# Performance work log

Hardware: AMD Instinct MI355X
Metric: run time of the kernel (lower is better)

Reference implementation:

```python
import jax, jax.numpy as jnp
import numpy as np

N = 100000; E = 1600000; G = 512; L = 1000
FXD = 4; FXT = 5; H = 64; NOUT = 2

def setup_inputs() -> dict:
    key = jax.random.key(0)
    ks = jax.random.split(key, 16)
    x = jax.random.normal(ks[0], (N, FXD), dtype=jnp.float32)
    edge_index = jax.random.randint(ks[1], (2, E), 0, N, dtype=jnp.int64)
    # contiguous, non-empty graph assignment (sorted)
    batch = jnp.minimum(jnp.arange(N, dtype=jnp.int64) // (N // G), G - 1)
    target = jax.random.normal(ks[2], (G, L, FXT), dtype=jnp.float32)
    def lin(k, fi, fo):
        s = 1.0 / np.sqrt(fi)
        k1, k2 = jax.random.split(k)
        return (jax.random.uniform(k1, (fi, fo), jnp.float32, -s, s),
                jax.random.uniform(k2, (fo,), jnp.float32, -s, s))
    W1, b1 = lin(ks[3], FXD, H)
    W2, b2 = lin(ks[4], H, 2 * H)
    Wg, bg = lin(ks[5], 2 * H, H)
    s = 1.0 / np.sqrt(FXT * 3)
    Wc = jax.random.uniform(ks[6], (H, FXT, 3), jnp.float32, -s, s)  # OIH
    bc = jax.random.uniform(ks[7], (H,), jnp.float32, -s, s)
    Wt, bt = lin(ks[8], H, H)
    Wf, bf = lin(ks[9], 2 * H, H)
    Wo, bo = lin(ks[10], H, NOUT)
    return dict(x=x, edge_index=edge_index, batch=batch, target=target,
                W1=W1, b1=b1, W2=W2, b2=b2, Wg=Wg, bg=bg,
                Wc=Wc, bc=bc, Wt=Wt, bt=bt, Wf=Wf, bf=bf, Wo=Wo, bo=bo)

def _gcn_prep(edge_index):
    # add self-loops, compute symmetric normalization (PyG gcn_norm)
    loops = jnp.arange(N, dtype=edge_index.dtype)
    row = jnp.concatenate([edge_index[0], loops])
    col = jnp.concatenate([edge_index[1], loops])
    deg = jax.ops.segment_sum(jnp.ones_like(col, dtype=jnp.float32), col, num_segments=N)
    dis = jnp.where(deg > 0, jax.lax.rsqrt(deg), 0.0)
    norm = dis[row] * dis[col]  # [E+N]
    return row, col, norm

def _gcn_conv(h, row, col, norm):
    # gather-scale-scatter aggregation
    msg = h[row] * norm[:, None]
    return jax.ops.segment_sum(msg, col, num_segments=N)

def reference(x, edge_index, batch, target, W1, b1, W2, b2, Wg, bg, Wc, bc, Wt, bt, Wf, bf, Wo, bo):
    row, col, norm = _gcn_prep(edge_index)
    h = jax.nn.relu(_gcn_conv(x @ W1, row, col, norm) + b1)
    h = jax.nn.relu(_gcn_conv(h @ W2, row, col, norm) + b2)
    g = jax.ops.segment_max(h, batch, num_segments=G)  # global_max_pool [G, 2H]
    g = g @ Wg + bg  # dropout = identity (eval)
    t = jnp.transpose(target, (0, 2, 1))  # [G, FXT, L]
    t = jax.lax.conv_general_dilated(t, Wc, (1,), 'VALID',
                                     dimension_numbers=('NCH', 'OIH', 'NCH')) + bc[None, :, None]
    t = jax.nn.relu(t)
    t = jnp.max(t, axis=-1)  # AdaptiveMaxPool1d(1) [G, H]
    t = t @ Wt + bt
    xc = jnp.concatenate([g, t], axis=1)
    xc = jax.nn.relu(xc @ Wf + bf)
    return xc @ Wo + bo
```

## Files before the change

### kernel.cpp

```cpp
#include <hip/hip_runtime.h>
#include <hip/hip_bf16.h>

constexpr int N   = 100000;
constexpr int E   = 1600000;
constexpr int G   = 512;
constexpr int L   = 1000;
constexpr int NPG = 195;

constexpr int SLOTS = 48;
constexpr int NR2   = 256;
constexpr int RS2   = 391;
constexpr int PCAP2 = 6912;
constexpr int BCH   = 4096;
constexpr int NBP   = (E + BCH - 1) / BCH;

typedef __attribute__((ext_vector_type(8))) short bf16x8;
typedef __attribute__((ext_vector_type(4))) float f32x4;

__device__ __forceinline__ float bf2f(__hip_bfloat16 b) { return __bfloat162float(b); }
__device__ __forceinline__ float lo_bf(unsigned v) { return __uint_as_float(v << 16); }
__device__ __forceinline__ float hi_bf(unsigned v) { return __uint_as_float(v & 0xFFFF0000u); }
__device__ __forceinline__ unsigned packbf2(float a, float b) {
    __hip_bfloat16 ha = __float2bfloat16(a), hb = __float2bfloat16(b);
    unsigned short ua = *(unsigned short*)&ha, ub = *(unsigned short*)&hb;
    return (unsigned)ua | ((unsigned)ub << 16);
}

struct SMPart { unsigned rec[BCH]; unsigned char rr[BCH];
                int cnt[NR2]; int base[NR2]; int cur[NR2]; };
struct SMConv { float tg[L * 5]; float pm[4 * 64]; };


__global__ void __launch_bounds__(256) k_part_conv(
        const int* __restrict__ row, const int* __restrict__ col,
        int* __restrict__ pcnt, unsigned* __restrict__ precs,
        const float* __restrict__ target, const float* __restrict__ Wc,
        const float* __restrict__ bc, float* __restrict__ tb,
        const float* __restrict__ W2, short* __restrict__ W2hi,
        short* __restrict__ W2lo) {
    __shared__ __align__(16) char smbuf[sizeof(SMPart) > sizeof(SMConv)
                                        ? sizeof(SMPart) : sizeof(SMConv)];
    int tid = threadIdx.x;
    int bid = blockIdx.x;
    if (bid < NBP) {
        SMPart& sp = *reinterpret_cast<SMPart*>(smbuf);
        sp.cnt[tid] = 0;
        __syncthreads();
        int e0 = bid * BCH;
        int nE = min(BCH, E - e0);
        for (int i = tid; i < nE; i += 256) {
            int c = __builtin_nontemporal_load(col + e0 + i);
            int r = __builtin_nontemporal_load(row + e0 + i);
            int rr = c / RS2;
            sp.rec[i] = ((unsigned)r << 9) | (unsigned)(c - rr * RS2);
            sp.rr[i] = (unsigned char)rr;
            atomicAdd(&sp.cnt[rr], 1);
        }
        __syncthreads();
        sp.base[tid] = atomicAdd(&pcnt[tid], sp.cnt[tid]);
        sp.cur[tid] = 0;
        __syncthreads();
        for (int i = tid; i < nE; i += 256) {
            int rr = sp.rr[i];
            int p = sp.base[rr] + atomicAdd(&sp.cur[rr], 1);
            if (p < PCAP2) precs[rr * PCAP2 + p] = sp.rec[i];
        }
    } else if (bid < NBP + G) {
        SMConv& sc = *reinterpret_cast<SMConv*>(smbuf);
        int gi = bid - NBP;
        const float* tsrc = target + (size_t)gi * (L * 5);
        for (int i = tid; i < L * 5; i += 256) sc.tg[i] = tsrc[i];
        __syncthreads();
        int co = tid & 63, rr = tid >> 6;
        float wc[15];
        #pragma unroll
        for (int j = 0; j < 15; j++) wc[j] = Wc[co * 15 + j];
        const float* tg = sc.tg;
        int p0 = rr * 250;
        int pend = min(p0 + 250, 998);
        float a0 = tg[p0 * 5 + 0], a1 = tg[p0 * 5 + 1], a2 = tg[p0 * 5 + 2],
              a3 = tg[p0 * 5 + 3], a4 = tg[p0 * 5 + 4];
        float b0 = tg[p0 * 5 + 5], b1 = tg[p0 * 5 + 6], b2 = tg[p0 * 5 + 7],
              b3 = tg[p0 * 5 + 8], b4 = tg[p0 * 5 + 9];
        float m = -1e30f;
        for (int p = p0; p < pend; p++) {
            const float* cp = &tg[(p + 2) * 5];
            float c0 = cp[0], c1 = cp[1], c2 = cp[2], c3 = cp[3], c4 = cp[4];
            float v = 0.0f;
            v = fmaf(a0, wc[0],  v); v = fmaf(b0, wc[1],  v); v = fmaf(c0, wc[2],  v);
            v = fmaf(a1, wc[3],  v); v = fmaf(b1, wc[4],  v); v = fmaf(c1, wc[5],  v);
            v = fmaf(a2, wc[6],  v); v = fmaf(b2, wc[7],  v); v = fmaf(c2, wc[8],  v);
            v = fmaf(a3, wc[9],  v); v = fmaf(b3, wc[10], v); v = fmaf(c3, wc[11], v);
            v = fmaf(a4, wc[12], v); v = fmaf(b4, wc[13], v); v = fmaf(c4, wc[14], v);
            m = fmaxf(m, v);
            a0 = b0; a1 = b1; a2 = b2; a3 = b3; a4 = b4;
            b0 = c0; b1 = c1; b2 = c2; b3 = c3; b4 = c4;
        }
        sc.pm[rr * 64 + co] = m;
        __syncthreads();
        if (tid < 64) {
            float mm = fmaxf(fmaxf(sc.pm[tid], sc.pm[64 + tid]),
                             fmaxf(sc.pm[128 + tid], sc.pm[192 + tid]));
            tb[gi * 64 + tid] = fmaxf(mm + bc[tid], 0.0f);
        }
    } else {
        int i = (bid - NBP - G) * 256 + tid;
        if (i < 64 * 128) {
            float w = W2[i];
            __hip_bfloat16 h = __float2bfloat16(w);
            float r = w - __bfloat162float(h);
            __hip_bfloat16 l = __float2bfloat16(r);
            W2hi[i] = *(short*)&h;
            W2lo[i] = *(short*)&l;
        }
    }
}


__global__ void __launch_bounds__(256) k_sort(
        const int* __restrict__ pcnt, const unsigned* __restrict__ precs,
        int* __restrict__ slots, int* __restrict__ cursor, float* __restrict__ dis) {
    __shared__ unsigned recs[PCAP2];
    __shared__ int hist[512], off[512], off2[512], ps[256];
    int tid = threadIdx.x;
    int rr = blockIdx.x;
    int cnt = min(pcnt[rr], PCAP2);
    hist[tid] = 0; hist[tid + 256] = 0;
    __syncthreads();
    const unsigned* pr = precs + rr * PCAP2;
    for (int i = tid; i < cnt; i += 256) {
        unsigned r = pr[i];
        recs[i] = r;
        atomicAdd(&hist[r & 511], 1);
    }
    __syncthreads();
    int h0 = hist[2 * tid], h1 = hist[2 * tid + 1];
    int s = h0 + h1;
    ps[tid] = s;
    __syncthreads();
    for (int d = 1; d < 256; d <<= 1) {
        int v = (tid >= d) ? ps[tid - d] : 0;
        __syncthreads();
        ps[tid] += v;
        __syncthreads();
    }
    int excl = ps[tid] - s;
    off[2 * tid] = excl;       off[2 * tid + 1] = excl + h0;
    off2[2 * tid] = excl;      off2[2 * tid + 1] = excl + h0;
    __syncthreads();
    for (int ln = tid; ln < RS2; ln += 256) {
        int n = rr * RS2 + ln;
        if (n < N) {
            int c = hist[ln];
            dis[n] = rsqrtf((float)c + 1.0f);
            cursor[n] = n * SLOTS + min(c, SLOTS);
        }
    }
    for (int i = tid; i < cnt; i += 256) {
        unsigned r = recs[i];
        int ln = (int)(r & 511u);
        int p = atomicAdd(&off2[ln], 1);
        int j = p - off[ln];
        if (j < SLOTS) slots[(rr * RS2 + ln) * SLOTS + j] = (int)(r >> 9);
    }
}


__global__ void __launch_bounds__(256) k_gxl1(
        const int* __restrict__ cursor, const int* __restrict__ slots,
        const float* __restrict__ dis, const float4* __restrict__ x,
        const float* __restrict__ W1, const float* __restrict__ b1,
        unsigned* __restrict__ h32) {
    __shared__ float ax[256][4];
    __shared__ float w1s[256];
    __shared__ float b1s[64];
    int tid = threadIdx.x;
    w1s[tid] = W1[tid];
    if (tid < 64) b1s[tid] = b1[tid];
    int nb = blockIdx.x * 256;
    int n = nb + tid;
    float4 a = make_float4(0.f, 0.f, 0.f, 0.f);
    if (n < N) {
        int s = n * SLOTS;
        int cnt = cursor[n] - s;
        float dn = dis[n];
        int j = 0;
        for (; j + 4 <= cnt; j += 4) {
            int s0 = slots[s + j], s1 = slots[s + j + 1],
                s2 = slots[s + j + 2], s3 = slots[s + j + 3];
            float w0 = dis[s0], w1 = dis[s1], w2 = dis[s2], w3 = dis[s3];
            float4 v0 = x[s0], v1 = x[s1], v2 = x[s2], v3 = x[s3];
            a.x = fmaf(v0.x, w0, a.x); a.y = fmaf(v0.y, w0, a.y);
            a.z = fmaf(v0.z, w0, a.z); a.w = fmaf(v0.w, w0, a.w);
            a.x = fmaf(v1.x, w1, a.x); a.y = fmaf(v1.y, w1, a.y);
            a.z = fmaf(v1.z, w1, a.z); a.w = fmaf(v1.w, w1, a.w);
            a.x = fmaf(v2.x, w2, a.x); a.y = fmaf(v2.y, w2, a.y);
            a.z = fmaf(v2.z, w2, a.z); a.w = fmaf(v2.w, w2, a.w);
            a.x = fmaf(v3.x, w3, a.x); a.y = fmaf(v3.y, w3, a.y);
            a.z = fmaf(v3.z, w3, a.z); a.w = fmaf(v3.w, w3, a.w);
        }
        for (; j < cnt; j++) {
            int sx = slots[s + j];
            float w = dis[sx];
            float4 v = x[sx];
            a.x = fmaf(v.x, w, a.x); a.y = fmaf(v.y, w, a.y);
            a.z = fmaf(v.z, w, a.z); a.w = fmaf(v.w, w, a.w);
        }
        float4 xs = x[n];
        float sl = dn * dn;
        a.x = fmaf(xs.x, sl, a.x * dn);
        a.y = fmaf(xs.y, sl, a.y * dn);
        a.z = fmaf(xs.z, sl, a.z * dn);
        a.w = fmaf(xs.w, sl, a.w * dn);
    }
    ax[tid][0] = a.x; ax[tid][1] = a.y; ax[tid][2] = a.z; ax[tid][3] = a.w;
    __syncthreads();
    int p = tid & 31, r0 = tid >> 5;
    int f0 = 2 * p, f1 = 2 * p + 1;
    float wA0 = w1s[f0],       wB0 = w1s[f1];
    float wA1 = w1s[64 + f0],  wB1 = w1s[64 + f1];
    float wA2 = w1s[128 + f0], wB2 = w1s[128 + f1];
    float wA3 = w1s[192 + f0], wB3 = w1s[192 + f1];
    float bb0 = b1s[f0], bb1 = b1s[f1];
    #pragma unroll 4
    for (int i = 0; i < 32; i++) {
        int ln = r0 + 8 * i;
        int node = nb + ln;
        if (node >= N) break;
        float v0 = bb0, v1 = bb1;
        float g0 = ax[ln][0], g1 = ax[ln][1], g2 = ax[ln][2], g3 = ax[ln][3];
        v0 = fmaf(g0, wA0, v0); v1 = fmaf(g0, wB0, v1);
        v0 = fmaf(g1, wA1, v0); v1 = fmaf(g1, wB1, v1);
        v0 = fmaf(g2, wA2, v0); v1 = fmaf(g2, wB2, v1);
        v0 = fmaf(g3, wA3, v0); v1 = fmaf(g3, wB3, v1);
        h32[(size_t)node * 32 + p] = packbf2(fmaxf(v0, 0.0f), fmaxf(v1, 0.0f));
    }
}


__global__ void __launch_bounds__(256) k_gather_h(
        const int* __restrict__ cursor, const int* __restrict__ slots,
        const float* __restrict__ dis, const unsigned* __restrict__ h32,
        unsigned* __restrict__ aggh32) {
    __shared__ int2 lsw[8][SLOTS];
    __shared__ int  lcnt[8];
    int tid = threadIdx.x;
    int nb = blockIdx.x * 8;
    if (tid < 8) {
        int node = nb + tid;
        lcnt[tid] = (node < N) ? (cursor[node] - node * SLOTS) : 0;
    }
    __syncthreads();
    for (int i = tid; i < 8 * SLOTS; i += 256) {
        int lo = i / SLOTS, j = i - lo * SLOTS;
        if (j < lcnt[lo]) {
            int src = slots[(nb + lo) * SLOTS + j];
            lsw[lo][j] = make_int2(src, __float_as_int(dis[src]));
        }
    }
    __syncthreads();
    int wid = tid >> 6, lane = tid & 63;
    int half = lane >> 5, li = lane & 31;
    int local = wid * 2 + half;
    int n = nb + local;
    if (n >= N) return;
    int cnt = lcnt[local];
    float dn = dis[n];
    float acc0 = 0.0f, acc1 = 0.0f;
    int j = 0;
    for (; j + 16 <= cnt; j += 16) {
        unsigned v[16]; float w[16];
        #pragma unroll
        for (int k = 0; k < 16; k++) {
            int2 e = lsw[local][j + k];
            v[k] = h32[(size_t)e.x * 32 + li];
            w[k] = __int_as_float(e.y);
        }
        #pragma unroll
        for (int k = 0; k < 16; k++) {
            acc0 = fmaf(w[k], lo_bf(v[k]), acc0);
            acc1 = fmaf(w[k], hi_bf(v[k]), acc1);
        }
    }
    for (; j + 4 <= cnt; j += 4) {
        unsigned v[4]; float w[4];
        #pragma unroll
        for (int k = 0; k < 4; k++) {
            int2 e = lsw[local][j + k];
            v[k] = h32[(size_t)e.x * 32 + li];
            w[k] = __int_as_float(e.y);
        }
        #pragma unroll
        for (int k = 0; k < 4; k++) {
            acc0 = fmaf(w[k], lo_bf(v[k]), acc0);
            acc1 = fmaf(w[k], hi_bf(v[k]), acc1);
        }
    }
    for (; j < cnt; j++) {
        int2 e = lsw[local][j];
        unsigned v = h32[(size_t)e.x * 32 + li];
        float w = __int_as_float(e.y);
        acc0 = fmaf(w, lo_bf(v), acc0);
        acc1 = fmaf(w, hi_bf(v), acc1);
    }
    unsigned sv = h32[(size_t)n * 32 + li];
    acc0 = fmaf(dn, lo_bf(sv), acc0) * dn;
    acc1 = fmaf(dn, hi_bf(sv), acc1) * dn;
    aggh32[(size_t)n * 32 + li] = packbf2(acc0, acc1);
}


__global__ void __launch_bounds__(256) k_mfma_pool(
        const __hip_bfloat16* __restrict__ aggh,
        const short* __restrict__ W2hi, const short* __restrict__ W2lo,
        const float* __restrict__ b2, const float* __restrict__ tb,
        const float* __restrict__ Wg, const float* __restrict__ bg,
        const float* __restrict__ Wt, const float* __restrict__ bt,
        const float* __restrict__ Wf, const float* __restrict__ bf,
        const float* __restrict__ Wo, const float* __restrict__ bo,
        float* __restrict__ out) {
    __shared__ float gvec[128], ts[64], g2s[64], t2s[64], xcs[64];
    int tid = threadIdx.x;
    int wid = tid >> 6, lane = tid & 63;
    int m = lane & 15, quad = lane >> 4;
    int gi = blockIdx.x;
    int n0 = gi * NPG;
    int n1 = (gi == G - 1) ? N : n0 + NPG;
    int cb0 = wid * 32, cb1 = cb0 + 16;
    bf16x8 bh[2][2], bl[2][2];
    #pragma unroll
    for (int t = 0; t < 2; t++) {
        int cb = cb0 + t * 16;
        #pragma unroll
        for (int ks = 0; ks < 2; ks++) {
            bf16x8 hh, ll;
            #pragma unroll
            for (int j = 0; j < 8; j++) {
                int k = ks * 32 + quad * 8 + j;
                hh[j] = W2hi[k * 128 + cb + m];
                ll[j] = W2lo[k * 128 + cb + m];
            }
            bh[t][ks] = hh; bl[t][ks] = ll;
        }
    }
    float bias0 = b2[cb0 + m], bias1 = b2[cb1 + m];
    const short* ah = (const short*)aggh;
    float mx0 = 0.0f, mx1 = 0.0f;
    bf16x8 a0, a1;
    {
        const short* p = ah + (size_t)(n0 + m) * 64 + quad * 8;
        a0 = *(const bf16x8*)p;
        a1 = *(const bf16x8*)(p + 32);
    }
    for (int bn = n0; bn < n1; bn += 16) {
        bf16x8 na0 = a0, na1 = a1;
        if (bn + 16 < n1) {
            const short* p = ah + (size_t)(bn + 16 + m) * 64 + quad * 8;
            na0 = *(const bf16x8*)p;
            na1 = *(const bf16x8*)(p + 32);
        }
        f32x4 acc0 = {0.f, 0.f, 0.f, 0.f};
        f32x4 acc1 = {0.f, 0.f, 0.f, 0.f};
        acc0 = __builtin_amdgcn_mfma_f32_16x16x32_bf16(a0, bh[0][0], acc0, 0, 0, 0);
        acc0 = __builtin_amdgcn_mfma_f32_16x16x32_bf16(a1, bh[0][1], acc0, 0, 0, 0);
        acc0 = __builtin_amdgcn_mfma_f32_16x16x32_bf16(a0, bl[0][0], acc0, 0, 0, 0);
        acc0 = __builtin_amdgcn_mfma_f32_16x16x32_bf16(a1, bl[0][1], acc0, 0, 0, 0);
        acc1 = __builtin_amdgcn_mfma_f32_16x16x32_bf16(a0, bh[1][0], acc1, 0, 0, 0);
        acc1 = __builtin_amdgcn_mfma_f32_16x16x32_bf16(a1, bh[1][1], acc1, 0, 0, 0);
        acc1 = __builtin_amdgcn_mfma_f32_16x16x32_bf16(a0, bl[1][0], acc1, 0, 0, 0);
        acc1 = __builtin_amdgcn_mfma_f32_16x16x32_bf16(a1, bl[1][1], acc1, 0, 0, 0);
        int rb = bn + quad * 4;
        #pragma unroll
        for (int r = 0; r < 4; r++) {
            float v0 = fmaxf(acc0[r] + bias0, 0.0f);
            float v1 = fmaxf(acc1[r] + bias1, 0.0f);
            if (rb + r < n1) {
                mx0 = fmaxf(mx0, v0);
                mx1 = fmaxf(mx1, v1);
            }
        }
        a0 = na0; a1 = na1;
    }
    mx0 = fmaxf(mx0, __shfl_xor(mx0, 16));
    mx0 = fmaxf(mx0, __shfl_xor(mx0, 32));
    mx1 = fmaxf(mx1, __shfl_xor(mx1, 16));
    mx1 = fmaxf(mx1, __shfl_xor(mx1, 32));
    if (quad == 0) {
        gvec[cb0 + m] = mx0;
        gvec[cb1 + m] = mx1;
    }
    __syncthreads();
    if (wid == 0) {
        ts[lane] = tb[gi * 64 + lane];
        float a = bg[lane];
        #pragma unroll 8
        for (int k = 0; k < 128; k++) a = fmaf(gvec[k], Wg[k * 64 + lane], a);
        float b = bt[lane];
        #pragma unroll 8
        for (int k = 0; k < 64; k++) b = fmaf(ts[k], Wt[k * 64 + lane], b);
        g2s[lane] = a;
        t2s[lane] = b;
        float c = bf[lane];
        #pragma unroll 8
        for (int k = 0; k < 64; k++) c = fmaf(g2s[k], Wf[k * 64 + lane], c);
        #pragma unroll 8
        for (int k = 0; k < 64; k++) c = fmaf(t2s[k], Wf[(64 + k) * 64 + lane], c);
        xcs[lane] = fmaxf(c, 0.0f);
        if (lane < 2) {
            float o = bo[lane];
            for (int k = 0; k < 64; k++) o = fmaf(xcs[k], Wo[k * 2 + lane], o);
            out[gi * 2 + lane] = o;
        }
    }
}


extern "C" void kernel_launch(void* const* d_in, const int* in_sizes, int n_in,
                              void* d_out, int out_size, void* d_ws, size_t ws_size,
                              hipStream_t stream) {
    const float* x      = (const float*)d_in[0];
    const int*   ei     = (const int*)d_in[1];
    const float* target = (const float*)d_in[3];
    const float* W1 = (const float*)d_in[4];
    const float* b1 = (const float*)d_in[5];
    const float* W2 = (const float*)d_in[6];
    const float* b2 = (const float*)d_in[7];
    const float* Wg = (const float*)d_in[8];
    const float* bg = (const float*)d_in[9];
    const float* Wc = (const float*)d_in[10];
    const float* bc = (const float*)d_in[11];
    const float* Wt = (const float*)d_in[12];
    const float* bt = (const float*)d_in[13];
    const float* Wf = (const float*)d_in[14];
    const float* bf = (const float*)d_in[15];
    const float* Wo = (const float*)d_in[16];
    const float* bo = (const float*)d_in[17];
    float* out = (float*)d_out;

    const int* row = ei;
    const int* col = ei + E;

    char* base = (char*)d_ws;
    size_t o = 0;
    auto alloc = [&](size_t bytes) -> void* {
        void* p = base + o;
        o = (o + bytes + 255) & ~(size_t)255;
        return p;
    };
    int*      cursor = (int*)     alloc((size_t)N * 4);
    float*    dis    = (float*)   alloc((size_t)N * 4);
    int*      slots  = (int*)     alloc((size_t)N * SLOTS * 4);
    int*      pcnt   = (int*)     alloc(NR2 * 4);
    unsigned* precs  = (unsigned*)alloc((size_t)NR2 * PCAP2 * 4);
    __hip_bfloat16* h    = (__hip_bfloat16*)alloc((size_t)N * 64 * 2);
    __hip_bfloat16* aggh = (__hip_bfloat16*)alloc((size_t)N * 64 * 2);
    short*    W2hi   = (short*)   alloc((size_t)64 * 128 * 2);
    short*    W2lo   = (short*)   alloc((size_t)64 * 128 * 2);
    float*    tb     = (float*)   alloc((size_t)G * 64 * 4);
    (void)    alloc(4096);

    (void)hipMemsetAsync(pcnt, 0, NR2 * 4, stream);
    k_part_conv<<<NBP + G + 32, 256, 0, stream>>>(row, col, pcnt, precs,
                                                  target, Wc, bc, tb,
                                                  W2, W2hi, W2lo);
    k_sort     <<<NR2, 256, 0, stream>>>(pcnt, precs, slots, cursor, dis);
    k_gxl1     <<<(N + 255) / 256, 256, 0, stream>>>(cursor, slots, dis,
                                                     (const float4*)x, W1, b1,
                                                     (unsigned*)h);
    k_gather_h <<<(N + 7) / 8, 256, 0, stream>>>(cursor, slots, dis,
                                                 (const unsigned*)h, (unsigned*)aggh);
    k_mfma_pool<<<G, 256, 0, stream>>>(aggh, W2hi, W2lo, b2, tb, Wg, bg, Wt, bt,
                                       Wf, bf, Wo, bo, out);
}
```

Before: 237.6 us.

## Simplify bucket sort to atomic slot fill and split layer-1 gather across 4 lanes

k_sort drops its LDS record staging, histogram prefix scan and second pass, and instead writes slots directly using a per-node atomic counter. The order of neighbours within a slot list now depends on atomic ordering, so floating-point summation order can vary between runs. k_gxl1 now assigns four threads per node, with each lane striding over the neighbour list, and combines the partial sums with xor shuffles. This gives four times as many blocks and is meant to shorten the serial per-thread gather and improve memory-level parallelism.

```diff
diff --git a/kernel.cpp b/kernel.cpp
--- a/kernel.cpp
+++ b/kernel.cpp
@@ -120,48 +120,27 @@
 __global__ void __launch_bounds__(256) k_sort(
         const int* __restrict__ pcnt, const unsigned* __restrict__ precs,
         int* __restrict__ slots, int* __restrict__ cursor, float* __restrict__ dis) {
-    __shared__ unsigned recs[PCAP2];
-    __shared__ int hist[512], off[512], off2[512], ps[256];
+    __shared__ int cnt2[RS2];
     int tid = threadIdx.x;
     int rr = blockIdx.x;
     int cnt = min(pcnt[rr], PCAP2);
-    hist[tid] = 0; hist[tid + 256] = 0;
+    for (int i = tid; i < RS2; i += 256) cnt2[i] = 0;
     __syncthreads();
     const unsigned* pr = precs + rr * PCAP2;
     for (int i = tid; i < cnt; i += 256) {
         unsigned r = pr[i];
-        recs[i] = r;
-        atomicAdd(&hist[r & 511], 1);
-    }
-    __syncthreads();
-    int h0 = hist[2 * tid], h1 = hist[2 * tid + 1];
-    int s = h0 + h1;
-    ps[tid] = s;
-    __syncthreads();
-    for (int d = 1; d < 256; d <<= 1) {
-        int v = (tid >= d) ? ps[tid - d] : 0;
-        __syncthreads();
-        ps[tid] += v;
-        __syncthreads();
-    }
-    int excl = ps[tid] - s;
-    off[2 * tid] = excl;       off[2 * tid + 1] = excl + h0;
-    off2[2 * tid] = excl;      off2[2 * tid + 1] = excl + h0;
+        int ln = (int)(r & 511u);
+        int j = atomicAdd(&cnt2[ln], 1);
+        if (j < SLOTS) slots[(rr * RS2 + ln) * SLOTS + j] = (int)(r >> 9);
+    }
     __syncthreads();
     for (int ln = tid; ln < RS2; ln += 256) {
         int n = rr * RS2 + ln;
         if (n < N) {
-            int c = hist[ln];
+            int c = cnt2[ln];
             dis[n] = rsqrtf((float)c + 1.0f);
             cursor[n] = n * SLOTS + min(c, SLOTS);
         }
-    }
-    for (int i = tid; i < cnt; i += 256) {
-        unsigned r = recs[i];
-        int ln = (int)(r & 511u);
-        int p = atomicAdd(&off2[ln], 1);
-        int j = p - off[ln];
-        if (j < SLOTS) slots[(rr * RS2 + ln) * SLOTS + j] = (int)(r >> 9);
     }
 }
 
@@ -171,49 +150,40 @@
         const float* __restrict__ dis, const float4* __restrict__ x,
         const float* __restrict__ W1, const float* __restrict__ b1,
         unsigned* __restrict__ h32) {
-    __shared__ float ax[256][4];
+    __shared__ float ax[64][4];
     __shared__ float w1s[256];
     __shared__ float b1s[64];
     int tid = threadIdx.x;
     w1s[tid] = W1[tid];
     if (tid < 64) b1s[tid] = b1[tid];
-    int nb = blockIdx.x * 256;
-    int n = nb + tid;
+    int nb = blockIdx.x * 64;
+    int ln = tid >> 2, sub = tid & 3;
+    int n = nb + ln;
     float4 a = make_float4(0.f, 0.f, 0.f, 0.f);
     if (n < N) {
         int s = n * SLOTS;
         int cnt = cursor[n] - s;
-        float dn = dis[n];
-        int j = 0;
-        for (; j + 4 <= cnt; j += 4) {
-            int s0 = slots[s + j], s1 = slots[s + j + 1],
-                s2 = slots[s + j + 2], s3 = slots[s + j + 3];
-            float w0 = dis[s0], w1 = dis[s1], w2 = dis[s2], w3 = dis[s3];
-            float4 v0 = x[s0], v1 = x[s1], v2 = x[s2], v3 = x[s3];
-            a.x = fmaf(v0.x, w0, a.x); a.y = fmaf(v0.y, w0, a.y);
-            a.z = fmaf(v0.z, w0, a.z); a.w = fmaf(v0.w, w0, a.w);
-            a.x = fmaf(v1.x, w1, a.x); a.y = fmaf(v1.y, w1, a.y);
-            a.z = fmaf(v1.z, w1, a.z); a.w = fmaf(v1.w, w1, a.w);
-            a.x = fmaf(v2.x, w2, a.x); a.y = fmaf(v2.y, w2, a.y);
-            a.z = fmaf(v2.z, w2, a.z); a.w = fmaf(v2.w, w2, a.w);
-            a.x = fmaf(v3.x, w3, a.x); a.y = fmaf(v3.y, w3, a.y);
-            a.z = fmaf(v3.z, w3, a.z); a.w = fmaf(v3.w, w3, a.w);
-        }
-        for (; j < cnt; j++) {
+        for (int j = sub; j < cnt; j += 4) {
             int sx = slots[s + j];
             float w = dis[sx];
             float4 v = x[sx];
             a.x = fmaf(v.x, w, a.x); a.y = fmaf(v.y, w, a.y);
             a.z = fmaf(v.z, w, a.z); a.w = fmaf(v.w, w, a.w);
         }
+    }
+    a.x += __shfl_xor(a.x, 1); a.y += __shfl_xor(a.y, 1);
+    a.z += __shfl_xor(a.z, 1); a.w += __shfl_xor(a.w, 1);
+    a.x += __shfl_xor(a.x, 2); a.y += __shfl_xor(a.y, 2);
+    a.z += __shfl_xor(a.z, 2); a.w += __shfl_xor(a.w, 2);
+    if (sub == 0 && n < N) {
+        float dn = dis[n];
+        float sl = dn * dn;
         float4 xs = x[n];
-        float sl = dn * dn;
-        a.x = fmaf(xs.x, sl, a.x * dn);
-        a.y = fmaf(xs.y, sl, a.y * dn);
-        a.z = fmaf(xs.z, sl, a.z * dn);
-        a.w = fmaf(xs.w, sl, a.w * dn);
-    }
-    ax[tid][0] = a.x; ax[tid][1] = a.y; ax[tid][2] = a.z; ax[tid][3] = a.w;
+        ax[ln][0] = fmaf(xs.x, sl, a.x * dn);
+        ax[ln][1] = fmaf(xs.y, sl, a.y * dn);
+        ax[ln][2] = fmaf(xs.z, sl, a.z * dn);
+        ax[ln][3] = fmaf(xs.w, sl, a.w * dn);
+    }
     __syncthreads();
     int p = tid & 31, r0 = tid >> 5;
     int f0 = 2 * p, f1 = 2 * p + 1;
@@ -222,13 +192,13 @@
     float wA2 = w1s[128 + f0], wB2 = w1s[128 + f1];
     float wA3 = w1s[192 + f0], wB3 = w1s[192 + f1];
     float bb0 = b1s[f0], bb1 = b1s[f1];
-    #pragma unroll 4
-    for (int i = 0; i < 32; i++) {
-        int ln = r0 + 8 * i;
-        int node = nb + ln;
+    #pragma unroll
+    for (int i = 0; i < 8; i++) {
+        int l2 = r0 + 8 * i;
+        int node = nb + l2;
         if (node >= N) break;
         float v0 = bb0, v1 = bb1;
-        float g0 = ax[ln][0], g1 = ax[ln][1], g2 = ax[ln][2], g3 = ax[ln][3];
+        float g0 = ax[l2][0], g1 = ax[l2][1], g2 = ax[l2][2], g3 = ax[l2][3];
         v0 = fmaf(g0, wA0, v0); v1 = fmaf(g0, wB0, v1);
         v0 = fmaf(g1, wA1, v0); v1 = fmaf(g1, wB1, v1);
         v0 = fmaf(g2, wA2, v0); v1 = fmaf(g2, wB2, v1);
@@ -464,9 +434,9 @@
                                                   target, Wc, bc, tb,
                                                   W2, W2hi, W2lo);
     k_sort     <<<NR2, 256, 0, stream>>>(pcnt, precs, slots, cursor, dis);
-    k_gxl1     <<<(N + 255) / 256, 256, 0, stream>>>(cursor, slots, dis,
-                                                     (const float4*)x, W1, b1,
-                                                     (unsigned*)h);
+    k_gxl1     <<<(N + 63) / 64, 256, 0, stream>>>(cursor, slots, dis,
+                                                   (const float4*)x, W1, b1,
+                                                   (unsigned*)h);
     k_gather_h <<<(N + 7) / 8, 256, 0, stream>>>(cursor, slots, dis,
                                                  (const unsigned*)h, (unsigned*)aggh);
     k_mfma_pool<<<G, 256, 0, stream>>>(aggh, W2hi, W2lo, b2, tb, Wg, bg, Wt, bt,
```

Measured after the change: 233.7 us. About the same (-1.7%).
